# Kernel tuning notes

Hardware: AMD Instinct MI355X
Metric: run time of the kernel (lower is better)

Reference implementation:

```python
import jax, jax.numpy as jnp
import numpy as np

D = 2048
H = 16
DH = D // H  # 128
B = 512
EPS = 1e-5


def _layernorm(x, g, b):
    m = jnp.mean(x, axis=-1, keepdims=True)
    v = jnp.mean((x - m) ** 2, axis=-1, keepdims=True)
    return (x - m) * jax.lax.rsqrt(v + EPS) * g + b


def setup_inputs() -> dict:
    key = jax.random.key(0)
    ks = jax.random.split(key, 16)
    s_in = 1.0 / np.sqrt(D)
    s_ff = 1.0 / np.sqrt(4 * D)
    return {
        "x": jax.random.normal(ks[0], (B, D), jnp.float32),
        # per-head q/k/v projections, stacked over heads: [H, D, DH]
        "Wq": jax.random.uniform(ks[1], (H, D, DH), jnp.float32, -s_in, s_in),
        "bq": jax.random.uniform(ks[2], (H, DH), jnp.float32, -s_in, s_in),
        "Wk": jax.random.uniform(ks[3], (H, D, DH), jnp.float32, -s_in, s_in),
        "bk": jax.random.uniform(ks[4], (H, DH), jnp.float32, -s_in, s_in),
        "Wv": jax.random.uniform(ks[5], (H, D, DH), jnp.float32, -s_in, s_in),
        "bv": jax.random.uniform(ks[6], (H, DH), jnp.float32, -s_in, s_in),
        "Wo": jax.random.uniform(ks[7], (D, D), jnp.float32, -s_in, s_in),
        "bo": jax.random.uniform(ks[8], (D,), jnp.float32, -s_in, s_in),
        "W1": jax.random.uniform(ks[9], (D, 4 * D), jnp.float32, -s_in, s_in),
        "b1": jax.random.uniform(ks[10], (4 * D,), jnp.float32, -s_in, s_in),
        "W2": jax.random.uniform(ks[11], (4 * D, D), jnp.float32, -s_ff, s_ff),
        "b2": jax.random.uniform(ks[12], (D,), jnp.float32, -s_ff, s_ff),
        "g1": jnp.ones((D,), jnp.float32),
        "be1": jnp.zeros((D,), jnp.float32),
        "g2": jnp.ones((D,), jnp.float32),
        "be2": jnp.zeros((D,), jnp.float32),
    }


def reference(x, Wq, bq, Wk, bk, Wv, bv, Wo, bo, W1, b1, W2, b2, g1, be1, g2, be2):
    # --- pre-norm attention branch ---
    h = _layernorm(x, g1, be1)                       # [B, D]
    q = jnp.einsum('bd,hde->bhe', h, Wq) + bq        # [B, H, DH]
    k = jnp.einsum('bd,hde->bhe', h, Wk) + bk
    v = jnp.einsum('bd,hde->bhe', h, Wv) + bv
    # outer-product 'attention' per sample: [B, H, DH, DH]
    attn = q[..., :, None] * k[..., None, :] / jnp.sqrt(jnp.float32(DH))
    attn = jax.nn.softmax(attn, axis=-1)
    o = jnp.einsum('bhij,bhj->bhi', attn, v)         # [B, H, DH]
    o = o.reshape(x.shape[0], H * DH)                # concat over heads
    x = x + o @ Wo + bo
    # --- pre-norm FFN branch ---
    h2 = _layernorm(x, g2, be2)
    x = x + jax.nn.relu(h2 @ W1 + b1) @ W2 + b2
    return x
```

## Files before the change

### kernel.cpp

```cpp
#include <hip/hip_runtime.h>
#include <hip/hip_bf16.h>
#include <math.h>


#define DDIM 2048
#define HHEADS 16
#define DHEAD 128
#define BROWS 512
#define LN_EPS 1e-5f

typedef __bf16 bf16x8_t __attribute__((ext_vector_type(8)));
typedef float f32x4_t __attribute__((ext_vector_type(4)));

#define GLD16(gptr, lptr)                                                     \
    __builtin_amdgcn_global_load_lds(                                         \
        (const __attribute__((address_space(1))) void*)(gptr),                \
        (__attribute__((address_space(3))) void*)(lptr), 16, 0, 0)

__global__ __launch_bounds__(256) void ln_kernel(const float* __restrict__ x,
                                                 const float* __restrict__ g,
                                                 const float* __restrict__ b,
                                                 __bf16* __restrict__ out) {
    const int row = blockIdx.x;
    const int tid = threadIdx.x;
    const float4* x4 = (const float4*)(x + (size_t)row * DDIM);
    float4 a = x4[2 * tid];
    float4 c = x4[2 * tid + 1];
    float s  = a.x + a.y + a.z + a.w + c.x + c.y + c.z + c.w;
    float s2 = a.x*a.x + a.y*a.y + a.z*a.z + a.w*a.w
             + c.x*c.x + c.y*c.y + c.z*c.z + c.w*c.w;
    #pragma unroll
    for (int off = 32; off > 0; off >>= 1) {
        s  += __shfl_down(s, off);
        s2 += __shfl_down(s2, off);
    }
    __shared__ float ps[4], ps2[4];
    __shared__ float mean_s, rstd_s;
    const int lane = tid & 63, w = tid >> 6;
    if (lane == 0) { ps[w] = s; ps2[w] = s2; }
    __syncthreads();
    if (tid == 0) {
        float S  = ps[0] + ps[1] + ps[2] + ps[3];
        float S2 = ps2[0] + ps2[1] + ps2[2] + ps2[3];
        float m  = S * (1.0f / DDIM);
        float var = S2 * (1.0f / DDIM) - m * m;
        mean_s = m;
        rstd_s = rsqrtf(var + LN_EPS);
    }
    __syncthreads();
    const float m = mean_s, r = rstd_s;
    const float4* g4 = (const float4*)g;
    const float4* b4 = (const float4*)b;
    float4 ga = g4[2 * tid], gb = g4[2 * tid + 1];
    float4 ba = b4[2 * tid], bb = b4[2 * tid + 1];
    bf16x8_t o;
    o[0] = (__bf16)((a.x - m) * r * ga.x + ba.x);
    o[1] = (__bf16)((a.y - m) * r * ga.y + ba.y);
    o[2] = (__bf16)((a.z - m) * r * ga.z + ba.z);
    o[3] = (__bf16)((a.w - m) * r * ga.w + ba.w);
    o[4] = (__bf16)((c.x - m) * r * gb.x + bb.x);
    o[5] = (__bf16)((c.y - m) * r * gb.y + bb.y);
    o[6] = (__bf16)((c.z - m) * r * gb.z + bb.z);
    o[7] = (__bf16)((c.w - m) * r * gb.w + bb.w);
    *(bf16x8_t*)(out + (size_t)row * DDIM + tid * 8) = o;
}

__global__ __launch_bounds__(256) void prep_kernel(
    const float* __restrict__ Wq, const float* __restrict__ Wk,
    const float* __restrict__ Wv, const float* __restrict__ Wo,
    const float* __restrict__ W1, const float* __restrict__ W2,
    const float* __restrict__ x, const float* __restrict__ g1,
    const float* __restrict__ be1,
    __bf16* __restrict__ bt_qkv, __bf16* __restrict__ Wot,
    __bf16* __restrict__ W1t, __bf16* __restrict__ W2t,
    __bf16* __restrict__ h) {
    __shared__ __align__(16) float tile[64 * 65];
    const int bid = blockIdx.x;
    const int t = threadIdx.x;
    if (bid < 12288) {
        const float* src;
        __bf16* dst;
        int R, C, r0, c0;
        if (bid < 3072) {
            const int z = bid >> 6, rem = bid & 63;
            const int which = z >> 4, hd = z & 15;
            src = ((which == 0) ? Wq : (which == 1) ? Wk : Wv) +
                  (size_t)hd * DDIM * DHEAD;
            dst = bt_qkv + (size_t)which * DDIM * DDIM +
                  (size_t)hd * DDIM * DHEAD;
            R = DDIM; C = DHEAD;
            c0 = (rem & 1) * 64; r0 = (rem >> 1) * 64;
        } else if (bid < 4096) {
            const int local = bid - 3072;
            src = Wo; dst = Wot; R = DDIM; C = DDIM;
            c0 = (local & 31) * 64; r0 = (local >> 5) * 64;
        } else if (bid < 8192) {
            const int local = bid - 4096;
            src = W1; dst = W1t; R = DDIM; C = 4 * DDIM;
            c0 = (local & 127) * 64; r0 = (local >> 7) * 64;
        } else {
            const int local = bid - 8192;
            src = W2; dst = W2t; R = 4 * DDIM; C = DDIM;
            c0 = (local & 31) * 64; r0 = (local >> 5) * 64;
        }
        const int rr = t >> 4, cc = (t & 15) * 4;
        #pragma unroll
        for (int p = 0; p < 4; p++) {
            const float4 v =
                *(const float4*)(src + (size_t)(r0 + rr + 16 * p) * C + c0 + cc);
            tile[(rr + 16 * p) * 65 + cc]     = v.x;
            tile[(rr + 16 * p) * 65 + cc + 1] = v.y;
            tile[(rr + 16 * p) * 65 + cc + 2] = v.z;
            tile[(rr + 16 * p) * 65 + cc + 3] = v.w;
        }
        __syncthreads();
        const int slot = t & 7;
        #pragma unroll
        for (int p = 0; p < 2; p++) {
            const int c = (t >> 3) + 32 * p;
            bf16x8_t o;
            #pragma unroll
            for (int j = 0; j < 8; j++)
                o[j] = (__bf16)tile[(slot * 8 + j) * 65 + c];
            *(bf16x8_t*)(dst + (size_t)(c0 + c) * R + r0 + slot * 8) = o;
        }
    } else {
        const int row = bid - 12288;
        const float4* x4 = (const float4*)(x + (size_t)row * DDIM);
        float4 a = x4[2 * t];
        float4 c = x4[2 * t + 1];
        float s  = a.x + a.y + a.z + a.w + c.x + c.y + c.z + c.w;
        float s2 = a.x*a.x + a.y*a.y + a.z*a.z + a.w*a.w
                 + c.x*c.x + c.y*c.y + c.z*c.z + c.w*c.w;
        #pragma unroll
        for (int off = 32; off > 0; off >>= 1) {
            s  += __shfl_down(s, off);
            s2 += __shfl_down(s2, off);
        }
        const int lane = t & 63, w = t >> 6;
        if (lane == 0) { tile[w] = s; tile[8 + w] = s2; }
        __syncthreads();
        if (t == 0) {
            float S  = tile[0] + tile[1] + tile[2] + tile[3];
            float S2 = tile[8] + tile[9] + tile[10] + tile[11];
            float m  = S * (1.0f / DDIM);
            float var = S2 * (1.0f / DDIM) - m * m;
            tile[16] = m;
            tile[17] = rsqrtf(var + LN_EPS);
        }
        __syncthreads();
        const float m = tile[16], r = tile[17];
        const float4* g4 = (const float4*)g1;
        const float4* b4 = (const float4*)be1;
        float4 ga = g4[2 * t], gb = g4[2 * t + 1];
        float4 ba = b4[2 * t], bb = b4[2 * t + 1];
        bf16x8_t o;
        o[0] = (__bf16)((a.x - m) * r * ga.x + ba.x);
        o[1] = (__bf16)((a.y - m) * r * ga.y + ba.y);
        o[2] = (__bf16)((a.z - m) * r * ga.z + ba.z);
        o[3] = (__bf16)((a.w - m) * r * ga.w + ba.w);
        o[4] = (__bf16)((c.x - m) * r * gb.x + bb.x);
        o[5] = (__bf16)((c.y - m) * r * gb.y + bb.y);
        o[6] = (__bf16)((c.z - m) * r * gb.z + bb.z);
        o[7] = (__bf16)((c.w - m) * r * gb.w + bb.w);
        *(bf16x8_t*)(h + (size_t)row * DDIM + t * 8) = o;
    }
}

template <int TM, int TN, int SPLITZ, int OUT_BF16, int RELU, int RES, int BIAS3>
__global__ __launch_bounds__(512) void gemm_bt(
    const __bf16* __restrict__ A, int K,
    const __bf16* __restrict__ Bt,
    const float* __restrict__ bias, const float* __restrict__ biasB,
    const float* __restrict__ biasC,
    const float* __restrict__ Res,
    void* __restrict__ Cout, int N) {
    constexpr int DEPTH = 4;
    constexpr int STG = (TM + TN) * 64;
    __shared__ __align__(16) __bf16 smem[DEPTH * STG];

    const int tid = threadIdx.x;
    const int w = tid >> 6, lane = tid & 63;

    const int gx = gridDim.x, gy = gridDim.y, gz = gridDim.z;
    int l = blockIdx.x + gx * (blockIdx.y + gy * blockIdx.z);
    const int xcd = l & 7;
    int i0 = l >> 3;
    const int by = i0 % gy; i0 /= gy;
    const int bz = i0 % gz; i0 /= gz;
    const int bx = xcd * (gx >> 3) + i0;

    const int m0 = by * TM, n0 = bx * TN;

    const int Kloc = K / SPLITZ;
    const int kb = bz * Kloc;
    const int NK = Kloc / 64;

    constexpr int NT = (TM + TN) / 8;
    constexpr int NI = NT / 8;

    const int srow = lane >> 3;
    const int sslot = (lane & 7) ^ srow;

    const __bf16* srcs[NI];
    int toff[NI];
    #pragma unroll
    for (int i = 0; i < NI; i++) {
        const int tt = w + 8 * i;
        toff[i] = tt * 512;
        const int r = tt * 8 + srow;
        srcs[i] = (r < TM)
                      ? A + (size_t)(m0 + r) * K + kb + sslot * 8
                      : Bt + (size_t)(n0 + r - TM) * K + kb + sslot * 8;
    }

    constexpr int MI = TM / 32, NJ = TN / 32;
    const int wg = w & 3, kh = w >> 2;
    const int wm = (wg >> 1) * (TM / 2), wn = (wg & 1) * (TN / 2);
    const int fm = lane & 15, quad = lane >> 4;
    const int f7 = fm & 7;

    const int sl = ((kh * 4 + quad) ^ f7) * 16;
    int aoff[MI], boff[NJ];
    #pragma unroll
    for (int i = 0; i < MI; i++)
        aoff[i] = (wm + 16 * i + fm) * 128 + sl;
    #pragma unroll
    for (int j = 0; j < NJ; j++)
        boff[j] = (TM + wn + 16 * j + fm) * 128 + sl;

    f32x4_t acc[MI][NJ] = {};

    #pragma unroll
    for (int d = 0; d < DEPTH; d++)
        #pragma unroll
        for (int i = 0; i < NI; i++)
            GLD16(srcs[i] + d * 64, smem + d * STG + toff[i]);

    for (int ks = 0; ks < NK; ks++) {
        const char* st = (const char*)smem + (ks % DEPTH) * (STG * 2);
        if (ks < NK - 2)
            asm volatile("s_waitcnt vmcnt(%0)\n\ts_barrier"
                         :: "i"((DEPTH - 2) * NI) : "memory");
        else if (ks == NK - 2)
            asm volatile("s_waitcnt vmcnt(%0)\n\ts_barrier"
                         :: "i"(NI) : "memory");
        else
            asm volatile("s_waitcnt vmcnt(0)\n\ts_barrier" ::: "memory");

        if (ks >= 1 && ks + DEPTH - 1 < NK) {
            __bf16* dst = smem + ((ks - 1) % DEPTH) * STG;
            #pragma unroll
            for (int i = 0; i < NI; i++)
                GLD16(srcs[i] + (size_t)(ks + DEPTH - 1) * 64, dst + toff[i]);
        }

        bf16x8_t a[MI], b[NJ];
        #pragma unroll
        for (int i = 0; i < MI; i++)
            a[i] = *(const bf16x8_t*)(st + aoff[i]);
        #pragma unroll
        for (int j = 0; j < NJ; j++)
            b[j] = *(const bf16x8_t*)(st + boff[j]);
        __builtin_amdgcn_s_setprio(1);
        #pragma unroll
        for (int i = 0; i < MI; i++)
            #pragma unroll
            for (int j = 0; j < NJ; j++)
                acc[i][j] = __builtin_amdgcn_mfma_f32_16x16x32_bf16(
                    a[i], b[j], acc[i][j], 0, 0, 0);
        __builtin_amdgcn_s_setprio(0);
    }

    char* mrg = (char*)smem + wg * (MI * NJ * 64 * 16);
    __syncthreads();
    if (kh == 1) {
        #pragma unroll
        for (int i = 0; i < MI; i++)
            #pragma unroll
            for (int j = 0; j < NJ; j++)
                *(f32x4_t*)(mrg + (((i * NJ + j) * 64) + lane) * 16) = acc[i][j];
    }
    __syncthreads();
    if (kh == 1) return;
    #pragma unroll
    for (int i = 0; i < MI; i++)
        #pragma unroll
        for (int j = 0; j < NJ; j++) {
            const f32x4_t p = *(const f32x4_t*)(mrg + (((i * NJ + j) * 64) + lane) * 16);
            acc[i][j][0] += p[0]; acc[i][j][1] += p[1];
            acc[i][j][2] += p[2]; acc[i][j][3] += p[3];
        }

    if (SPLITZ > 1) {
        float* P = (float*)Cout + (size_t)bz * (gy * TM) * N;
        #pragma unroll
        for (int i = 0; i < MI; i++)
            #pragma unroll
            for (int j = 0; j < NJ; j++) {
                const int col = n0 + wn + 16 * j + fm;
                #pragma unroll
                for (int r = 0; r < 4; r++) {
                    const int row = m0 + wm + 16 * i + quad * 4 + r;
                    P[(size_t)row * N + col] = acc[i][j][r];
                }
            }
    } else {
        const float* bp = bias;
        if (BIAS3) {
            const int seg = n0 >> 11;
            bp = (seg == 0) ? bias : (seg == 1) ? biasB : biasC;
        }
        #pragma unroll
        for (int i = 0; i < MI; i++)
            #pragma unroll
            for (int j = 0; j < NJ; j++) {
                const int col = n0 + wn + 16 * j + fm;
                const float bcol = BIAS3 ? bp[col & 2047] : bp[col];
                #pragma unroll
                for (int r = 0; r < 4; r++) {
                    const int row = m0 + wm + 16 * i + quad * 4 + r;
                    float val = acc[i][j][r] + bcol;
                    if (RES) val += Res[(size_t)row * N + col];
                    if (RELU) val = fmaxf(val, 0.0f);
                    if (OUT_BF16)
                        ((__bf16*)Cout)[(size_t)row * N + col] = (__bf16)val;
                    else
                        ((float*)Cout)[(size_t)row * N + col] = val;
                }
            }
    }
}

template <int NS>
__global__ __launch_bounds__(256) void reduce_splitk(
    const float* __restrict__ part, const float* __restrict__ Res,
    const float* __restrict__ bias, float* __restrict__ out) {
    const int idx = blockIdx.x * 256 + threadIdx.x;
    const float4 b4 = ((const float4*)bias)[idx & 511];
    float4 r = ((const float4*)Res)[idx];
    #pragma unroll
    for (int s = 0; s < NS; s++) {
        const float4 p = ((const float4*)part)[(size_t)s * 262144 + idx];
        r.x += p.x; r.y += p.y; r.z += p.z; r.w += p.w;
    }
    r.x += b4.x; r.y += b4.y; r.z += b4.z; r.w += b4.w;
    ((float4*)out)[idx] = r;
}

__global__ __launch_bounds__(128) void attn_kernel(
    const __bf16* __restrict__ qkv, __bf16* __restrict__ o) {
    const int bh = blockIdx.x;
    const int b = bh >> 4, h = bh & 15;
    const size_t base = (size_t)b * (3 * DDIM) + h * DHEAD;
    const int tid = threadIdx.x;
    __shared__ float ks[DHEAD], vs[DHEAD];
    ks[tid] = (float)qkv[base + DDIM + tid];
    vs[tid] = (float)qkv[base + 2 * DDIM + tid];
    __syncthreads();
    const float a = (float)qkv[base + tid] * 0.08838834764831845f;
    float den = 0.0f, num = 0.0f;
    #pragma unroll 8
    for (int j = 0; j < DHEAD; j++) {
        float e = __expf(a * ks[j]);
        den += e;
        num += e * vs[j];
    }
    o[(size_t)b * DDIM + h * DHEAD + tid] = (__bf16)(num / den);
}

extern "C" void kernel_launch(void* const* d_in, const int* in_sizes, int n_in,
                              void* d_out, int out_size, void* d_ws, size_t ws_size,
                              hipStream_t stream) {
    const float* x   = (const float*)d_in[0];
    const float* Wq  = (const float*)d_in[1];
    const float* bq  = (const float*)d_in[2];
    const float* Wk  = (const float*)d_in[3];
    const float* bk  = (const float*)d_in[4];
    const float* Wv  = (const float*)d_in[5];
    const float* bv  = (const float*)d_in[6];
    const float* Wo  = (const float*)d_in[7];
    const float* bo  = (const float*)d_in[8];
    const float* W1  = (const float*)d_in[9];
    const float* b1  = (const float*)d_in[10];
    const float* W2  = (const float*)d_in[11];
    const float* b2  = (const float*)d_in[12];
    const float* g1  = (const float*)d_in[13];
    const float* be1 = (const float*)d_in[14];
    const float* g2  = (const float*)d_in[15];
    const float* be2 = (const float*)d_in[16];
    float* out = (float*)d_out;

    char* base = (char*)d_ws;
    __bf16* bt_qkv = (__bf16*)(base + 0);
    __bf16* Wot    = (__bf16*)(base + 25165824);
    __bf16* W1t    = (__bf16*)(base + 33554432);
    __bf16* W2t    = (__bf16*)(base + 67108864);
    __bf16* h      = (__bf16*)(base + 100663296);
    __bf16* qkv    = (__bf16*)(base + 102760448);
    __bf16* ob     = (__bf16*)(base + 109051904);
    float*  x1     = (float*)(base + 111149056);
    __bf16* h2     = (__bf16*)(base + 115343360);
    __bf16* t      = (__bf16*)(base + 117440512);
    float*  w2P    = (float*)(base + 125829120);

    prep_kernel<<<12800, 256, 0, stream>>>(Wq, Wk, Wv, Wo, W1, W2, x, g1, be1,
                                           bt_qkv, Wot, W1t, W2t, h);

    gemm_bt<128, 128, 1, 1, 0, 0, 1><<<dim3(48, 4), 512, 0, stream>>>(
        h, DDIM, bt_qkv, bq, bk, bv, nullptr, qkv, 3 * DDIM);

    attn_kernel<<<BROWS * HHEADS, 128, 0, stream>>>(qkv, ob);

    gemm_bt<64, 64, 1, 0, 0, 1, 0><<<dim3(32, 8), 512, 0, stream>>>(
        ob, DDIM, Wot, bo, nullptr, nullptr, x, x1, DDIM);

    ln_kernel<<<BROWS, 256, 0, stream>>>(x1, g2, be2, h2);

    gemm_bt<128, 128, 1, 1, 1, 0, 0><<<dim3(64, 4), 512, 0, stream>>>(
        h2, DDIM, W1t, b1, nullptr, nullptr, nullptr, t, 4 * DDIM);

    gemm_bt<128, 128, 4, 0, 0, 0, 0><<<dim3(16, 4, 4), 512, 0, stream>>>(
        t, 4 * DDIM, W2t, nullptr, nullptr, nullptr, nullptr, w2P, DDIM);

    reduce_splitk<4><<<1024, 256, 0, stream>>>(w2P, x1, b2, out);
}
```

Measured before the change: 353.4 us.

## Rework weight transpose-convert to 256x64 tiles with swizzled bf16 LDS staging

The weight transpose/convert stage now processes 256x64 tiles per block instead of 64x64. It converts to bf16 before writing into a swizzled LDS buffer and writes output in 16-byte chunks, so far fewer blocks are launched and each moves more data. The QKV GEMM tile shape changes to 64x192 with a 32x8 grid, so its bias selection now happens per column because a tile can span two of the Q/K/V bias segments. The aim is to cut the cost of the per-call weight conversion pass and to use more CUs in the QKV GEMM. The global reads are now scalar strided per column rather than float4.

```diff
diff --git a/kernel.cpp b/kernel.cpp
--- a/kernel.cpp
+++ b/kernel.cpp
@@ -10,6 +10,7 @@
 #define LN_EPS 1e-5f
 
 typedef __bf16 bf16x8_t __attribute__((ext_vector_type(8)));
+typedef __bf16 bf16x4_t __attribute__((ext_vector_type(4)));
 typedef float f32x4_t __attribute__((ext_vector_type(4)));
 
 #define GLD16(gptr, lptr)                                                     \
@@ -74,58 +75,64 @@
     __bf16* __restrict__ bt_qkv, __bf16* __restrict__ Wot,
     __bf16* __restrict__ W1t, __bf16* __restrict__ W2t,
     __bf16* __restrict__ h) {
-    __shared__ __align__(16) float tile[64 * 65];
+    __shared__ __align__(16) char shmem[32768];
     const int bid = blockIdx.x;
     const int t = threadIdx.x;
-    if (bid < 12288) {
+    if (bid < 3072) {
         const float* src;
         __bf16* dst;
         int R, C, r0, c0;
-        if (bid < 3072) {
-            const int z = bid >> 6, rem = bid & 63;
-            const int which = z >> 4, hd = z & 15;
+        if (bid < 768) {
+            const int mat = bid >> 4, rem = bid & 15;
+            const int which = mat >> 4, hd = mat & 15;
             src = ((which == 0) ? Wq : (which == 1) ? Wk : Wv) +
                   (size_t)hd * DDIM * DHEAD;
             dst = bt_qkv + (size_t)which * DDIM * DDIM +
                   (size_t)hd * DDIM * DHEAD;
             R = DDIM; C = DHEAD;
-            c0 = (rem & 1) * 64; r0 = (rem >> 1) * 64;
-        } else if (bid < 4096) {
-            const int local = bid - 3072;
+            r0 = (rem >> 1) * 256; c0 = (rem & 1) * 64;
+        } else if (bid < 1024) {
+            const int local = bid - 768;
             src = Wo; dst = Wot; R = DDIM; C = DDIM;
-            c0 = (local & 31) * 64; r0 = (local >> 5) * 64;
-        } else if (bid < 8192) {
-            const int local = bid - 4096;
+            r0 = (local >> 5) * 256; c0 = (local & 31) * 64;
+        } else if (bid < 2048) {
+            const int local = bid - 1024;
             src = W1; dst = W1t; R = DDIM; C = 4 * DDIM;
-            c0 = (local & 127) * 64; r0 = (local >> 7) * 64;
+            r0 = (local >> 7) * 256; c0 = (local & 127) * 64;
         } else {
-            const int local = bid - 8192;
+            const int local = bid - 2048;
             src = W2; dst = W2t; R = 4 * DDIM; C = DDIM;
-            c0 = (local & 31) * 64; r0 = (local >> 5) * 64;
-        }
-        const int rr = t >> 4, cc = (t & 15) * 4;
-        #pragma unroll
-        for (int p = 0; p < 4; p++) {
-            const float4 v =
-                *(const float4*)(src + (size_t)(r0 + rr + 16 * p) * C + c0 + cc);
-            tile[(rr + 16 * p) * 65 + cc]     = v.x;
-            tile[(rr + 16 * p) * 65 + cc + 1] = v.y;
-            tile[(rr + 16 * p) * 65 + cc + 2] = v.z;
-            tile[(rr + 16 * p) * 65 + cc + 3] = v.w;
+            r0 = (local >> 5) * 256; c0 = (local & 31) * 64;
+        }
+        const int w = t >> 6, l = t & 63;
+        const int c = l;
+        const int sw = (c & 31) << 4;
+        const float* sp = src + (size_t)r0 * C + c0 + c;
+        #pragma unroll
+        for (int g = 0; g < 16; g++) {
+            const int rl = g * 16 + w * 4;
+            const float v0 = sp[(size_t)(rl + 0) * C];
+            const float v1 = sp[(size_t)(rl + 1) * C];
+            const float v2 = sp[(size_t)(rl + 2) * C];
+            const float v3 = sp[(size_t)(rl + 3) * C];
+            bf16x4_t u;
+            u[0] = (__bf16)v0; u[1] = (__bf16)v1;
+            u[2] = (__bf16)v2; u[3] = (__bf16)v3;
+            *(bf16x4_t*)(shmem + c * 512 + ((rl * 2) ^ sw)) = u;
         }
         __syncthreads();
-        const int slot = t & 7;
-        #pragma unroll
-        for (int p = 0; p < 2; p++) {
-            const int c = (t >> 3) + 32 * p;
-            bf16x8_t o;
-            #pragma unroll
-            for (int j = 0; j < 8; j++)
-                o[j] = (__bf16)tile[(slot * 8 + j) * 65 + c];
-            *(bf16x8_t*)(dst + (size_t)(c0 + c) * R + r0 + slot * 8) = o;
+        #pragma unroll
+        for (int q = 0; q < 8; q++) {
+            const int co = w * 16 + (q & 3) * 4 + ((l >> 4) & 3);
+            const int chunk = (l & 15) + (q >> 2) * 16;
+            const int swo = (co & 31) << 4;
+            const bf16x8_t o =
+                *(const bf16x8_t*)(shmem + co * 512 + ((chunk * 16) ^ swo));
+            *(bf16x8_t*)(dst + (size_t)(c0 + co) * R + r0 + chunk * 8) = o;
         }
     } else {
-        const int row = bid - 12288;
+        float* tile = (float*)shmem;
+        const int row = bid - 3072;
         const float4* x4 = (const float4*)(x + (size_t)row * DDIM);
         float4 a = x4[2 * t];
         float4 c = x4[2 * t + 1];
@@ -306,17 +313,19 @@
                 }
             }
     } else {
-        const float* bp = bias;
-        if (BIAS3) {
-            const int seg = n0 >> 11;
-            bp = (seg == 0) ? bias : (seg == 1) ? biasB : biasC;
-        }
         #pragma unroll
         for (int i = 0; i < MI; i++)
             #pragma unroll
             for (int j = 0; j < NJ; j++) {
                 const int col = n0 + wn + 16 * j + fm;
-                const float bcol = BIAS3 ? bp[col & 2047] : bp[col];
+                float bcol;
+                if (BIAS3) {
+                    const float* bp = (col < 2048) ? bias
+                                    : (col < 4096) ? biasB : biasC;
+                    bcol = bp[col & 2047];
+                } else {
+                    bcol = bias[col];
+                }
                 #pragma unroll
                 for (int r = 0; r < 4; r++) {
                     const int row = m0 + wm + 16 * i + quad * 4 + r;
@@ -404,10 +413,10 @@
     __bf16* t      = (__bf16*)(base + 117440512);
     float*  w2P    = (float*)(base + 125829120);
 
-    prep_kernel<<<12800, 256, 0, stream>>>(Wq, Wk, Wv, Wo, W1, W2, x, g1, be1,
-                                           bt_qkv, Wot, W1t, W2t, h);
-
-    gemm_bt<128, 128, 1, 1, 0, 0, 1><<<dim3(48, 4), 512, 0, stream>>>(
+    prep_kernel<<<3584, 256, 0, stream>>>(Wq, Wk, Wv, Wo, W1, W2, x, g1, be1,
+                                          bt_qkv, Wot, W1t, W2t, h);
+
+    gemm_bt<64, 192, 1, 1, 0, 0, 1><<<dim3(32, 8), 512, 0, stream>>>(
         h, DDIM, bt_qkv, bq, bk, bv, nullptr, qkv, 3 * DDIM);
 
     attn_kernel<<<BROWS * HHEADS, 128, 0, stream>>>(qkv, ob);
```

After: 351.3 us. About the same (-0.6%).
